# Optimization experiments

Measured on AMD Instinct MI355X. Metric: run time of the kernel, lower is better.

The kernel has to match this reference:

```python
import jax, jax.numpy as jnp
import numpy as np
from jax import lax

SHARED = 512
THRESH = 1.0   # LifNeuron threshold from source
DECAY = 0.9    # assumed LIF membrane decay (LifNeuron source not provided)


def spike(u):
    return (u >= 0.0).astype(u.dtype)


def lif(x):
    # Leaky integrate-and-fire over the time axis. x: (B, T, D) -> spikes (B, T, D)
    def step(mem, xt):
        mem = DECAY * mem + xt
        s = spike(mem - THRESH)
        return mem - s * THRESH, s
    x_t = jnp.swapaxes(x, 0, 1)  # (T, B, D)
    _, spikes = lax.scan(step, jnp.zeros((x.shape[0], x.shape[2]), x.dtype), x_t)
    return jnp.swapaxes(spikes, 0, 1)


def setup_inputs() -> dict:
    key = jax.random.key(0)
    ks = jax.random.split(key, 10)
    B, T, S = 2, 32, 64
    Dv, Da = 768, 512
    TENSOR_DIM = (SHARED + 1) ** 2  # 263169

    def lin_w(k, fan_in, fan_out):
        # torch.nn.Linear default init scale ~ 1/sqrt(fan_in)
        return (jax.random.normal(k, (fan_out, fan_in), jnp.float32)
                * np.float32(1.0 / np.sqrt(fan_in)))

    return {
        "vision": jax.random.uniform(ks[0], (B, T, S, Dv), jnp.float32),
        "audio": jax.random.uniform(ks[1], (B, T, S, Da), jnp.float32),
        "vw1": lin_w(ks[2], Dv, SHARED), "vb1": jnp.zeros((SHARED,), jnp.float32),
        "vw2": lin_w(ks[3], SHARED, SHARED), "vb2": jnp.zeros((SHARED,), jnp.float32),
        "aw1": lin_w(ks[4], Da, SHARED), "ab1": jnp.zeros((SHARED,), jnp.float32),
        "aw2": lin_w(ks[5], SHARED, SHARED), "ab2": jnp.zeros((SHARED,), jnp.float32),
        "fw1": lin_w(ks[6], TENSOR_DIM, 2 * SHARED), "fb1": jnp.zeros((2 * SHARED,), jnp.float32),
        "fw2": lin_w(ks[7], 2 * SHARED, SHARED), "fb2": jnp.zeros((SHARED,), jnp.float32),
    }


def reference(vision, audio, vw1, vb1, vw2, vb2, aw1, ab1, aw2, ab2,
              fw1, fb1, fw2, fb2):
    def unimodal(x, w1, b1, w2, b2):
        p = x.mean(axis=2)  # (B, T, D_mod) - pool over spike/token axis
        h = jax.nn.relu(jnp.einsum('btd,hd->bth', p, w1) + b1)
        h = jnp.einsum('bth,oh->bto', h, w2) + b2  # (B, T, SHARED)
        ones = jnp.ones(h.shape[:-1] + (1,), h.dtype)
        return jnp.concatenate([h, ones], axis=-1)  # (B, T, SHARED+1)

    a = unimodal(vision, vw1, vb1, vw2, vb2)
    b = unimodal(audio, aw1, ab1, aw2, ab2)
    B, T, _ = a.shape
    # outer-product tensor fusion: (B, T, (SHARED+1)^2)
    tp = jnp.einsum('btd,bte->btde', a, b).reshape(B, T, -1)
    h = jax.nn.relu(jnp.einsum('btk,ok->bto', tp, fw1) + fb1)
    fused = jnp.einsum('bto,fo->btf', h, fw2) + fb2  # (B, T, SHARED)
    return lif(fused)
```

## Files before the change

### kernel.cpp

```cpp
#include <hip/hip_runtime.h>

#define AB 513
#define TD 263169
#define TILE 16416

typedef float f4 __attribute__((ext_vector_type(4)));
typedef float f32x4 __attribute__((ext_vector_type(4)));
typedef short bf16x8 __attribute__((ext_vector_type(8)));
typedef int i32x4 __attribute__((ext_vector_type(4)));
#define GAS __attribute__((address_space(1)))
#define LAS __attribute__((address_space(3)))

__global__ __launch_bounds__(256) void pool_kernel(
    const float* __restrict__ vx, const float* __restrict__ ax,
    float* __restrict__ pvT, float* __restrict__ paT)
{
    const int isA = (blockIdx.x >= 64);
    const int bt = blockIdx.x & 63;
    const float* x = isA ? ax : vx;
    float* pT = isA ? paT : pvT;
    const int D = isA ? 512 : 768;
    const int nd4 = D >> 2;
    const int tid = threadIdx.x;
    if (tid < nd4) {
        f4 s0 = {0.f, 0.f, 0.f, 0.f}, s1 = s0, s2 = s0, s3 = s0;
        const float* xp = x + (size_t)bt * 64 * D + tid * 4;
        #pragma unroll 4
        for (int ss = 0; ss < 64; ss += 4) {
            s0 += *(const f4*)(xp + (size_t)ss * D);
            s1 += *(const f4*)(xp + (size_t)(ss + 1) * D);
            s2 += *(const f4*)(xp + (size_t)(ss + 2) * D);
            s3 += *(const f4*)(xp + (size_t)(ss + 3) * D);
        }
        const f4 s = ((s0 + s1) + (s2 + s3)) * 0.015625f;
        #pragma unroll
        for (int q = 0; q < 4; ++q) pT[(tid * 4 + q) * 64 + bt] = s[q];
    }
}

__global__ __launch_bounds__(512) void mlp1_kernel(
    const float* __restrict__ pvT, const float* __restrict__ paT,
    const float* __restrict__ vw1, const float* __restrict__ vb1,
    const float* __restrict__ aw1, const float* __restrict__ ab1,
    float* __restrict__ h1vT, float* __restrict__ h1aT)
{
    const int isA = (blockIdx.x >= 64);
    const int D = isA ? 512 : 768;
    const float* pT = isA ? paT : pvT;
    const float* w1 = isA ? aw1 : vw1;
    const float* b1 = isA ? ab1 : vb1;
    float* h1T = isA ? h1aT : h1vT;
    const int tid = threadIdx.x, lane = tid & 63, w = tid >> 6;
    const int h = (blockIdx.x & 63) * 8 + w;
    const float* wr = w1 + (size_t)h * D;

    float a0 = 0.f, a1 = 0.f, a2 = 0.f, a3 = 0.f;
    for (int d = 0; d < D; d += 16) {
        const f4 w0 = *(const f4*)(wr + d);
        const f4 w1v = *(const f4*)(wr + d + 4);
        const f4 w2v = *(const f4*)(wr + d + 8);
        const f4 w3v = *(const f4*)(wr + d + 12);
        #pragma unroll
        for (int q = 0; q < 4; ++q) {
            a0 = fmaf(w0[q],  pT[(d + q) * 64 + lane], a0);
            a1 = fmaf(w1v[q], pT[(d + 4 + q) * 64 + lane], a1);
            a2 = fmaf(w2v[q], pT[(d + 8 + q) * 64 + lane], a2);
            a3 = fmaf(w3v[q], pT[(d + 12 + q) * 64 + lane], a3);
        }
    }
    h1T[h * 64 + lane] = fmaxf((a0 + a1) + (a2 + a3) + b1[h], 0.f);
}

__global__ __launch_bounds__(512) void mlp2_kernel(
    const float* __restrict__ h1vT, const float* __restrict__ h1aT,
    const float* __restrict__ vw2, const float* __restrict__ vb2,
    const float* __restrict__ aw2, const float* __restrict__ ab2,
    float* __restrict__ aTout, float* __restrict__ bTout)
{
    const int isA = (blockIdx.x >= 64);
    const float* hT = isA ? h1aT : h1vT;
    const float* w2 = isA ? aw2 : vw2;
    const float* b2 = isA ? ab2 : vb2;
    float* outT = isA ? bTout : aTout;
    const int tid = threadIdx.x, lane = tid & 63, w = tid >> 6;
    const int h = (blockIdx.x & 63) * 8 + w;
    const float* wr = w2 + (size_t)h * 512;

    float a0 = 0.f, a1 = 0.f, a2 = 0.f, a3 = 0.f;
    for (int d = 0; d < 512; d += 16) {
        const f4 w0 = *(const f4*)(wr + d);
        const f4 w1v = *(const f4*)(wr + d + 4);
        const f4 w2v = *(const f4*)(wr + d + 8);
        const f4 w3v = *(const f4*)(wr + d + 12);
        #pragma unroll
        for (int q = 0; q < 4; ++q) {
            a0 = fmaf(w0[q],  hT[(d + q) * 64 + lane], a0);
            a1 = fmaf(w1v[q], hT[(d + 4 + q) * 64 + lane], a1);
            a2 = fmaf(w2v[q], hT[(d + 8 + q) * 64 + lane], a2);
            a3 = fmaf(w3v[q], hT[(d + 12 + q) * 64 + lane], a3);
        }
    }
    outT[h * 64 + lane] = (a0 + a1) + (a2 + a3) + b2[h];
    if ((blockIdx.x & 63) == 0 && tid < 64) outT[512 * 64 + tid] = 1.0f;
}

__global__ __launch_bounds__(256) void aprep_kernel(
    const float* __restrict__ aT,
    short* __restrict__ aF1, short* __restrict__ aF2, short* __restrict__ aF3)
{
    const int t = blockIdx.x * 256 + threadIdx.x;
    const int l = t & 63, mt = (t >> 6) & 3, kt = t >> 8;
    const int m = mt * 16 + (l & 15);
    const int kbase = kt * 32 + ((l >> 4) << 3);
    const int obase = ((kt * 4 + mt) * 64 + l) * 8;
    #pragma unroll
    for (int i = 0; i < 8; ++i) {
        const float v = aT[(size_t)(kbase + i) * 64 + m];
        const unsigned u = __float_as_uint(v);
        const float r1 = v - __uint_as_float(u & 0xFFFF0000u);
        const unsigned u1 = __float_as_uint(r1);
        const float r2 = r1 - __uint_as_float(u1 & 0xFFFF0000u);
        const unsigned u2 = __float_as_uint(r2);
        aF1[obase + i] = (short)(u >> 16);
        aF2[obase + i] = (short)(u1 >> 16);
        aF3[obase + i] = (short)(u2 >> 16);
    }
}

__global__ __launch_bounds__(512, 1) void bilinear_kernel(
    const float* __restrict__ fw1,
    const float* __restrict__ fb1,
    const float* __restrict__ aT,
    const float* __restrict__ bT,
    const short* __restrict__ aF1, const short* __restrict__ aF2,
    const short* __restrict__ aF3,
    float* __restrict__ hbufT)
{
    __shared__ float lds[33344];
    float* const buf0 = lds;
    float* const buf1 = lds + 16448;
    float* const ldsdump = lds + 32896;

    const int tid = threadIdx.x;
    const int l = tid & 63, w = tid >> 6;
    const int o = blockIdx.x;
    const float* __restrict__ W = fw1 + (size_t)o * TD;
    const int we0 = w * 64;
    const int lq = l >> 4, ln = l & 15;

    #define STAGE(bufb_, c_)                                                   \
        do {                                                                   \
            const float* csrc_ = W + (size_t)(c_) * TILE;                      \
            _Pragma("unroll")                                                  \
            for (int is_ = 0; is_ < 8; ++is_) {                                \
                __builtin_amdgcn_global_load_lds(                              \
                    (const GAS unsigned*)(const void*)(csrc_ + w * 2048 + is_ * 256 + l * 4), \
                    (LAS unsigned*)(void*)((bufb_) + w * 2048 + is_ * 256), 16, 0, 0); \
            }                                                                  \
            {       \
                const float* rs_ = csrc_ + 16384 + (l & 31);                   \
                float* rd_ = (w == 0) ? ((bufb_) + 16384) : (ldsdump + (w - 1) * 64); \
                __builtin_amdgcn_global_load_lds(                              \
                    (const GAS unsigned*)(const void*)rs_,                     \
                    (LAS unsigned*)(void*)rd_, 4, 0, 0);                       \
            }                                                                  \
        } while (0)

    #define LOADA(A1r, A2r, A3r, kt_)                                          \
        do {                                                                   \
            _Pragma("unroll")                                                  \
            for (int mt_ = 0; mt_ < 4; ++mt_) {                                \
                const int fb_ = (((kt_) * 4 + mt_) * 64 + l) * 8;              \
                A1r[mt_] = *(const bf16x8*)(aF1 + fb_);                        \
                A2r[mt_] = *(const bf16x8*)(aF2 + fb_);                        \
                A3r[mt_] = *(const bf16x8*)(aF3 + fb_);                        \
            }                                                                  \
        } while (0)

    #define COMPUTE(wb_, A1r, A2r, A3r)                                        \
        do {                                                                   \
            _Pragma("unroll")                                                  \
            for (int nt = 0; nt < 4; ++nt) {                                   \
                unsigned u0[8], u1[8], u2[8];                                  \
                _Pragma("unroll")                                              \
                for (int i = 0; i < 8; ++i) {                                  \
                    const float v = (wb_)[(lq * 8 + i) * 513 + we0 + nt * 16 + ln]; \
                    u0[i] = __float_as_uint(v);                                \
                    const float r1 = v - __uint_as_float(u0[i] & 0xFFFF0000u); \
                    u1[i] = __float_as_uint(r1);                               \
                    const float r2 = r1 - __uint_as_float(u1[i] & 0xFFFF0000u);\
                    u2[i] = __float_as_uint(r2);                               \
                }                                                              \
                i32x4 p1, p2, p3;                                              \
                _Pragma("unroll")                                              \
                for (int j = 0; j < 4; ++j) {                                  \
                    p1[j] = (int)((u0[2 * j + 1] & 0xFFFF0000u) | (u0[2 * j] >> 16)); \
                    p2[j] = (int)((u1[2 * j + 1] & 0xFFFF0000u) | (u1[2 * j] >> 16)); \
                    p3[j] = (int)((u2[2 * j + 1] & 0xFFFF0000u) | (u2[2 * j] >> 16)); \
                }                                                              \
                const bf16x8 B1 = __builtin_bit_cast(bf16x8, p1);              \
                const bf16x8 B2 = __builtin_bit_cast(bf16x8, p2);              \
                const bf16x8 B3 = __builtin_bit_cast(bf16x8, p3);              \
                _Pragma("unroll")                                              \
                for (int mt = 0; mt < 4; ++mt) {                               \
                    acc[mt][nt] = __builtin_amdgcn_mfma_f32_16x16x32_bf16(A1r[mt], B1, acc[mt][nt], 0, 0, 0); \
                    acc[mt][nt] = __builtin_amdgcn_mfma_f32_16x16x32_bf16(A1r[mt], B2, acc[mt][nt], 0, 0, 0); \
                    acc[mt][nt] = __builtin_amdgcn_mfma_f32_16x16x32_bf16(A2r[mt], B1, acc[mt][nt], 0, 0, 0); \
                    acc[mt][nt] = __builtin_amdgcn_mfma_f32_16x16x32_bf16(A2r[mt], B2, acc[mt][nt], 0, 0, 0); \
                    acc[mt][nt] = __builtin_amdgcn_mfma_f32_16x16x32_bf16(A1r[mt], B3, acc[mt][nt], 0, 0, 0); \
                    acc[mt][nt] = __builtin_amdgcn_mfma_f32_16x16x32_bf16(A3r[mt], B1, acc[mt][nt], 0, 0, 0); \
                }                                                              \
            }                                                                  \
        } while (0)

    f32x4 acc[4][4];
    #pragma unroll
    for (int mt = 0; mt < 4; ++mt)
        #pragma unroll
        for (int nt = 0; nt < 4; ++nt)
            acc[mt][nt] = (f32x4){0.f, 0.f, 0.f, 0.f};

    bf16x8 Aa1[4], Aa2[4], Aa3[4], Ab1[4], Ab2[4], Ab3[4];

    STAGE(buf0, 0);
    LOADA(Aa1, Aa2, Aa3, 0);
    STAGE(buf1, 1);

    #pragma unroll 1
    for (int it = 0; it < 7; ++it) {
        asm volatile("s_waitcnt vmcnt(9)" ::: "memory");
        __builtin_amdgcn_s_barrier();
        LOADA(Ab1, Ab2, Ab3, 2 * it + 1);
        COMPUTE(buf0, Aa1, Aa2, Aa3);
        __builtin_amdgcn_s_barrier();
        STAGE(buf0, 2 * it + 2);

        asm volatile("s_waitcnt vmcnt(9)" ::: "memory");
        __builtin_amdgcn_s_barrier();
        LOADA(Aa1, Aa2, Aa3, 2 * it + 2);
        COMPUTE(buf1, Ab1, Ab2, Ab3);
        __builtin_amdgcn_s_barrier();
        STAGE(buf1, 2 * it + 3);
    }
    asm volatile("s_waitcnt vmcnt(9)" ::: "memory");
    __builtin_amdgcn_s_barrier();
    LOADA(Ab1, Ab2, Ab3, 15);
    COMPUTE(buf0, Aa1, Aa2, Aa3);
    __builtin_amdgcn_s_barrier();
    asm volatile("s_waitcnt vmcnt(0)" ::: "memory");
    __builtin_amdgcn_s_barrier();
    COMPUTE(buf1, Ab1, Ab2, Ab3);

    float ysum[4][4];
    #pragma unroll
    for (int mt = 0; mt < 4; ++mt)
        #pragma unroll
        for (int r = 0; r < 4; ++r) ysum[mt][r] = 0.f;
    #pragma unroll
    for (int mt = 0; mt < 4; ++mt) {
        const int bt0 = mt * 16 + lq * 4;
        #pragma unroll
        for (int nt = 0; nt < 4; ++nt) {
            const int e = we0 + nt * 16 + ln;
            const f4 bv = *(const f4*)(bT + (size_t)e * 64 + bt0);
            #pragma unroll
            for (int r = 0; r < 4; ++r)
                ysum[mt][r] = fmaf(acc[mt][nt][r], bv[r], ysum[mt][r]);
        }
    }
    #pragma unroll
    for (int mt = 0; mt < 4; ++mt)
        #pragma unroll
        for (int r = 0; r < 4; ++r) {
            float v = ysum[mt][r];
            v += __shfl_xor(v, 1, 64);
            v += __shfl_xor(v, 2, 64);
            v += __shfl_xor(v, 4, 64);
            v += __shfl_xor(v, 8, 64);
            ysum[mt][r] = v;
        }
    __syncthreads();
    if (ln == 0) {
        #pragma unroll
        for (int mt = 0; mt < 4; ++mt)
            #pragma unroll
            for (int r = 0; r < 4; ++r)
                buf0[w * 64 + mt * 16 + lq * 4 + r] = ysum[mt][r];
    }

    {
        float s0 = 0.f, s1 = 0.f, s2 = 0.f, s3 = 0.f;
        #pragma unroll 4
        for (int k = 0; k < 64; k += 4) {
            s0 = fmaf(aT[(size_t)(we0 + k) * 64 + l], W[(size_t)(we0 + k) * AB + 512], s0);
            s1 = fmaf(aT[(size_t)(we0 + k + 1) * 64 + l], W[(size_t)(we0 + k + 1) * AB + 512], s1);
            s2 = fmaf(aT[(size_t)(we0 + k + 2) * 64 + l], W[(size_t)(we0 + k + 2) * AB + 512], s2);
            s3 = fmaf(aT[(size_t)(we0 + k + 3) * 64 + l], W[(size_t)(we0 + k + 3) * AB + 512], s3);
        }
        #pragma unroll 4
        for (int k = 0; k < 64; k += 4) {
            s0 = fmaf(W[(size_t)512 * AB + we0 + k], bT[(size_t)(we0 + k) * 64 + l], s0);
            s1 = fmaf(W[(size_t)512 * AB + we0 + k + 1], bT[(size_t)(we0 + k + 1) * 64 + l], s1);
            s2 = fmaf(W[(size_t)512 * AB + we0 + k + 2], bT[(size_t)(we0 + k + 2) * 64 + l], s2);
            s3 = fmaf(W[(size_t)512 * AB + we0 + k + 3], bT[(size_t)(we0 + k + 3) * 64 + l], s3);
        }
        buf0[512 + w * 64 + l] = (s0 + s1) + (s2 + s3);
    }

    __syncthreads();

    if (w == 0) {
        float t2 = 0.f;
        #pragma unroll
        for (int k = 0; k < 8; ++k)
            t2 += buf0[k * 64 + l] + buf0[512 + k * 64 + l];
        t2 += W[(size_t)512 * AB + 512] + fb1[o];
        hbufT[(size_t)o * 64 + l] = fmaxf(t2, 0.f);
    }
    #undef STAGE
    #undef LOADA
    #undef COMPUTE
}

__global__ __launch_bounds__(512) void fuse2_kernel(
    const float* __restrict__ hbufT,
    const float* __restrict__ fw2,
    const float* __restrict__ fb2,
    float* __restrict__ fused)
{
    const int tid = threadIdx.x, lane = tid & 63, w = tid >> 6;
    #pragma unroll
    for (int k = 0; k < 2; ++k) {
        const int f = blockIdx.x * 16 + w * 2 + k;
        const float* wr = fw2 + (size_t)f * 1024;
        float a0 = 0.f, a1 = 0.f, a2 = 0.f, a3 = 0.f;
        for (int o = 0; o < 1024; o += 16) {
            const f4 w0 = *(const f4*)(wr + o);
            const f4 w1v = *(const f4*)(wr + o + 4);
            const f4 w2v = *(const f4*)(wr + o + 8);
            const f4 w3v = *(const f4*)(wr + o + 12);
            #pragma unroll
            for (int q = 0; q < 4; ++q) {
                a0 = fmaf(w0[q],  hbufT[(o + q) * 64 + lane], a0);
                a1 = fmaf(w1v[q], hbufT[(o + 4 + q) * 64 + lane], a1);
                a2 = fmaf(w2v[q], hbufT[(o + 8 + q) * 64 + lane], a2);
                a3 = fmaf(w3v[q], hbufT[(o + 12 + q) * 64 + lane], a3);
            }
        }
        fused[lane * 512 + f] = (a0 + a1) + (a2 + a3) + fb2[f];
    }
}

__global__ __launch_bounds__(256) void lif_kernel(
    const float* __restrict__ fused,
    float* __restrict__ out)
{
    const int idx = blockIdx.x * 256 + threadIdx.x;
    if (idx >= 1024) return;
    const int b = idx >> 9, dd = idx & 511;
    float mem = 0.f;
    for (int t = 0; t < 32; ++t) {
        const size_t off = ((size_t)(b * 32 + t) * 512) + dd;
        mem = 0.9f * mem + fused[off];
        const float s = (mem >= 1.0f) ? 1.0f : 0.0f;
        out[off] = s;
        mem -= s;
    }
}

extern "C" void kernel_launch(void* const* d_in, const int* in_sizes, int n_in,
                              void* d_out, int out_size, void* d_ws, size_t ws_size,
                              hipStream_t stream) {
    const float* vision = (const float*)d_in[0];
    const float* audio  = (const float*)d_in[1];
    const float* vw1 = (const float*)d_in[2];
    const float* vb1 = (const float*)d_in[3];
    const float* vw2 = (const float*)d_in[4];
    const float* vb2 = (const float*)d_in[5];
    const float* aw1 = (const float*)d_in[6];
    const float* ab1 = (const float*)d_in[7];
    const float* aw2 = (const float*)d_in[8];
    const float* ab2 = (const float*)d_in[9];
    const float* fw1 = (const float*)d_in[10];
    const float* fb1 = (const float*)d_in[11];
    const float* fw2 = (const float*)d_in[12];
    const float* fb2 = (const float*)d_in[13];
    float* out = (float*)d_out;

    float* ws    = (float*)d_ws;
    float* pvT   = ws;
    float* paT   = pvT + 768 * 64;
    float* h1vT  = paT + 512 * 64;
    float* h1aT  = h1vT + 512 * 64;
    float* aT    = h1aT + 512 * 64;
    float* bT    = aT + AB * 64;
    float* hbufT = bT + AB * 64;
    float* fused = hbufT + 1024 * 64;
    short* aF1   = (short*)(fused + 64 * 512);
    short* aF2   = aF1 + 32768;
    short* aF3   = aF2 + 32768;

    pool_kernel<<<128, 256, 0, stream>>>(vision, audio, pvT, paT);
    mlp1_kernel<<<128, 512, 0, stream>>>(pvT, paT, vw1, vb1, aw1, ab1, h1vT, h1aT);
    mlp2_kernel<<<128, 512, 0, stream>>>(h1vT, h1aT, vw2, vb2, aw2, ab2, aT, bT);
    aprep_kernel<<<16, 256, 0, stream>>>(aT, aF1, aF2, aF3);
    bilinear_kernel<<<1024, 512, 0, stream>>>(fw1, fb1, aT, bT, aF1, aF2, aF3, hbufT);
    fuse2_kernel<<<32, 512, 0, stream>>>(hbufT, fw2, fb2, fused);
    lif_kernel<<<4, 256, 0, stream>>>(fused, out);
}
```

Measured before the change: 423.2 us.

## Pipeline bilinear kernel with triple-buffered LDS ring for weights and A fragments

```diff
diff --git a/kernel.cpp b/kernel.cpp
--- a/kernel.cpp
+++ b/kernel.cpp
@@ -2,7 +2,6 @@
 
 #define AB 513
 #define TD 263169
-#define TILE 16416
 
 typedef float f4 __attribute__((ext_vector_type(4)));
 typedef float f32x4 __attribute__((ext_vector_type(4)));
@@ -15,27 +14,21 @@
     const float* __restrict__ vx, const float* __restrict__ ax,
     float* __restrict__ pvT, float* __restrict__ paT)
 {
-    const int isA = (blockIdx.x >= 64);
-    const int bt = blockIdx.x & 63;
-    const float* x = isA ? ax : vx;
-    float* pT = isA ? paT : pvT;
-    const int D = isA ? 512 : 768;
-    const int nd4 = D >> 2;
-    const int tid = threadIdx.x;
-    if (tid < nd4) {
-        f4 s0 = {0.f, 0.f, 0.f, 0.f}, s1 = s0, s2 = s0, s3 = s0;
-        const float* xp = x + (size_t)bt * 64 * D + tid * 4;
-        #pragma unroll 4
-        for (int ss = 0; ss < 64; ss += 4) {
-            s0 += *(const f4*)(xp + (size_t)ss * D);
-            s1 += *(const f4*)(xp + (size_t)(ss + 1) * D);
-            s2 += *(const f4*)(xp + (size_t)(ss + 2) * D);
-            s3 += *(const f4*)(xp + (size_t)(ss + 3) * D);
-        }
-        const f4 s = ((s0 + s1) + (s2 + s3)) * 0.015625f;
-        #pragma unroll
-        for (int q = 0; q < 4; ++q) pT[(tid * 4 + q) * 64 + bt] = s[q];
-    }
+    int b = blockIdx.x;
+    const float* x; float* pT; int D, bt, dc;
+    if (b < 192) { x = vx; pT = pvT; D = 768; bt = b / 3; dc = b % 3; }
+    else { b -= 192; x = ax; pT = paT; D = 512; bt = b >> 1; dc = b & 1; }
+    const int d = dc * 256 + threadIdx.x;
+    const float* xp = x + (size_t)bt * 64 * D + d;
+    float s0 = 0.f, s1 = 0.f, s2 = 0.f, s3 = 0.f;
+    #pragma unroll 4
+    for (int ss = 0; ss < 64; ss += 4) {
+        s0 += xp[(size_t)ss * D];
+        s1 += xp[(size_t)(ss + 1) * D];
+        s2 += xp[(size_t)(ss + 2) * D];
+        s3 += xp[(size_t)(ss + 3) * D];
+    }
+    pT[d * 64 + bt] = ((s0 + s1) + (s2 + s3)) * 0.015625f;
 }
 
 __global__ __launch_bounds__(512) void mlp1_kernel(
@@ -106,13 +99,13 @@
 
 __global__ __launch_bounds__(256) void aprep_kernel(
     const float* __restrict__ aT,
-    short* __restrict__ aF1, short* __restrict__ aF2, short* __restrict__ aF3)
+    short* __restrict__ aFc)
 {
     const int t = blockIdx.x * 256 + threadIdx.x;
     const int l = t & 63, mt = (t >> 6) & 3, kt = t >> 8;
     const int m = mt * 16 + (l & 15);
     const int kbase = kt * 32 + ((l >> 4) << 3);
-    const int obase = ((kt * 4 + mt) * 64 + l) * 8;
+    const int cb = kt * 12 + mt * 3;
     #pragma unroll
     for (int i = 0; i < 8; ++i) {
         const float v = aT[(size_t)(kbase + i) * 64 + m];
@@ -121,9 +114,9 @@
         const unsigned u1 = __float_as_uint(r1);
         const float r2 = r1 - __uint_as_float(u1 & 0xFFFF0000u);
         const unsigned u2 = __float_as_uint(r2);
-        aF1[obase + i] = (short)(u >> 16);
-        aF2[obase + i] = (short)(u1 >> 16);
-        aF3[obase + i] = (short)(u2 >> 16);
+        aFc[((size_t)(cb + 0) * 64 + l) * 8 + i] = (short)(u >> 16);
+        aFc[((size_t)(cb + 1) * 64 + l) * 8 + i] = (short)(u1 >> 16);
+        aFc[((size_t)(cb + 2) * 64 + l) * 8 + i] = (short)(u2 >> 16);
     }
 }
 
@@ -132,59 +125,74 @@
     const float* __restrict__ fb1,
     const float* __restrict__ aT,
     const float* __restrict__ bT,
-    const short* __restrict__ aF1, const short* __restrict__ aF2,
-    const short* __restrict__ aF3,
+    const short* __restrict__ aFc,
     float* __restrict__ hbufT)
 {
-    __shared__ float lds[33344];
-    float* const buf0 = lds;
-    float* const buf1 = lds + 16448;
-    float* const ldsdump = lds + 32896;
+    __shared__ float wring[3][8192];
+    __shared__ short aring[3][6144];
+    __shared__ float adump[256];
 
     const int tid = threadIdx.x;
     const int l = tid & 63, w = tid >> 6;
     const int o = blockIdx.x;
     const float* __restrict__ W = fw1 + (size_t)o * TD;
-    const int we0 = w * 64;
     const int lq = l >> 4, ln = l & 15;
 
-    #define STAGE(bufb_, c_)                                                   \
+    #define STAGE_W(e_)                                                        \
         do {                                                                   \
-            const float* csrc_ = W + (size_t)(c_) * TILE;                      \
+            const int ee_ = (e_), kt_ = ee_ >> 1, eh_ = ee_ & 1, en_ = ee_ % 3;\
             _Pragma("unroll")                                                  \
-            for (int is_ = 0; is_ < 8; ++is_) {                                \
+            for (int rr_ = 0; rr_ < 4; ++rr_) {                                \
+                const int r_ = w * 4 + rr_;                                    \
                 __builtin_amdgcn_global_load_lds(                              \
-                    (const GAS unsigned*)(const void*)(csrc_ + w * 2048 + is_ * 256 + l * 4), \
-                    (LAS unsigned*)(void*)((bufb_) + w * 2048 + is_ * 256), 16, 0, 0); \
-            }                                                                  \
-            {       \
-                const float* rs_ = csrc_ + 16384 + (l & 31);                   \
-                float* rd_ = (w == 0) ? ((bufb_) + 16384) : (ldsdump + (w - 1) * 64); \
-                __builtin_amdgcn_global_load_lds(                              \
-                    (const GAS unsigned*)(const void*)rs_,                     \
-                    (LAS unsigned*)(void*)rd_, 4, 0, 0);                       \
+                    (const GAS unsigned*)(const void*)(W + (size_t)(kt_ * 32 + r_) * AB + 256 * eh_ + l * 4), \
+                    (LAS unsigned*)(void*)(&wring[en_][r_ * 256]), 16, 0, 0);  \
             }                                                                  \
         } while (0)
 
-    #define LOADA(A1r, A2r, A3r, kt_)                                          \
+    #define STAGE_A(kt_)                                                       \
         do {                                                                   \
+            const int kk_ = (kt_), en_ = kk_ % 3;                              \
+            const int c0_ = (w < 4) ? (2 * w) : (4 + w);                       \
+            const short* s0_ = aFc + ((size_t)kk_ * 12 + c0_) * 512;           \
+            __builtin_amdgcn_global_load_lds(                                  \
+                (const GAS unsigned*)(const void*)(s0_ + l * 8),               \
+                (LAS unsigned*)(void*)(&aring[en_][c0_ * 512]), 16, 0, 0);     \
+            if (w < 4) {                                                       \
+                const int c1_ = 2 * w + 1;                                     \
+                const short* s1_ = aFc + ((size_t)kk_ * 12 + c1_) * 512;       \
+                __builtin_amdgcn_global_load_lds(                              \
+                    (const GAS unsigned*)(const void*)(s1_ + l * 8),           \
+                    (LAS unsigned*)(void*)(&aring[en_][c1_ * 512]), 16, 0, 0); \
+            } else {                                                           \
+                const short* s1_ = aFc + (size_t)kk_ * 12 * 512;               \
+                __builtin_amdgcn_global_load_lds(                              \
+                    (const GAS unsigned*)(const void*)(s1_ + l * 2),           \
+                    (LAS unsigned*)(void*)(adump), 4, 0, 0);                   \
+            }                                                                  \
+        } while (0)
+
+    #define LOADA_LDS(kt_)                                                     \
+        do {                                                                   \
+            const int en_ = (kt_) % 3;                                         \
             _Pragma("unroll")                                                  \
             for (int mt_ = 0; mt_ < 4; ++mt_) {                                \
-                const int fb_ = (((kt_) * 4 + mt_) * 64 + l) * 8;              \
-                A1r[mt_] = *(const bf16x8*)(aF1 + fb_);                        \
-                A2r[mt_] = *(const bf16x8*)(aF2 + fb_);                        \
-                A3r[mt_] = *(const bf16x8*)(aF3 + fb_);                        \
+                A1[mt_] = *(const bf16x8*)&aring[en_][(mt_ * 3 + 0) * 512 + l * 8]; \
+                A2[mt_] = *(const bf16x8*)&aring[en_][(mt_ * 3 + 1) * 512 + l * 8]; \
+                A3[mt_] = *(const bf16x8*)&aring[en_][(mt_ * 3 + 2) * 512 + l * 8]; \
             }                                                                  \
         } while (0)
 
-    #define COMPUTE(wb_, A1r, A2r, A3r)                                        \
+    #define COMPUTE(e_, EHC)                                                   \
         do {                                                                   \
+            const float* __restrict__ wb_ = &wring[(e_) % 3][0];               \
             _Pragma("unroll")                                                  \
-            for (int nt = 0; nt < 4; ++nt) {                                   \
+            for (int ntl = 0; ntl < 2; ++ntl) {                                \
+                const int col_ = 32 * w + 16 * ntl + ln;                       \
                 unsigned u0[8], u1[8], u2[8];                                  \
                 _Pragma("unroll")                                              \
                 for (int i = 0; i < 8; ++i) {                                  \
-                    const float v = (wb_)[(lq * 8 + i) * 513 + we0 + nt * 16 + ln]; \
+                    const float v = wb_[(lq * 8 + i) * 256 + col_];            \
                     u0[i] = __float_as_uint(v);                                \
                     const float r1 = v - __uint_as_float(u0[i] & 0xFFFF0000u); \
                     u1[i] = __float_as_uint(r1);                               \
@@ -203,12 +211,12 @@
                 const bf16x8 B3 = __builtin_bit_cast(bf16x8, p3);              \
                 _Pragma("unroll")                                              \
                 for (int mt = 0; mt < 4; ++mt) {                               \
-                    acc[mt][nt] = __builtin_amdgcn_mfma_f32_16x16x32_bf16(A1r[mt], B1, acc[mt][nt], 0, 0, 0); \
-                    acc[mt][nt] = __builtin_amdgcn_mfma_f32_16x16x32_bf16(A1r[mt], B2, acc[mt][nt], 0, 0, 0); \
-                    acc[mt][nt] = __builtin_amdgcn_mfma_f32_16x16x32_bf16(A2r[mt], B1, acc[mt][nt], 0, 0, 0); \
-                    acc[mt][nt] = __builtin_amdgcn_mfma_f32_16x16x32_bf16(A2r[mt], B2, acc[mt][nt], 0, 0, 0); \
-                    acc[mt][nt] = __builtin_amdgcn_mfma_f32_16x16x32_bf16(A1r[mt], B3, acc[mt][nt], 0, 0, 0); \
-                    acc[mt][nt] = __builtin_amdgcn_mfma_f32_16x16x32_bf16(A3r[mt], B1, acc[mt][nt], 0, 0, 0); \
+                    acc[mt][(EHC) * 2 + ntl] = __builtin_amdgcn_mfma_f32_16x16x32_bf16(A1[mt], B1, acc[mt][(EHC) * 2 + ntl], 0, 0, 0); \
+                    acc[mt][(EHC) * 2 + ntl] = __builtin_amdgcn_mfma_f32_16x16x32_bf16(A1[mt], B2, acc[mt][(EHC) * 2 + ntl], 0, 0, 0); \
+                    acc[mt][(EHC) * 2 + ntl] = __builtin_amdgcn_mfma_f32_16x16x32_bf16(A2[mt], B1, acc[mt][(EHC) * 2 + ntl], 0, 0, 0); \
+                    acc[mt][(EHC) * 2 + ntl] = __builtin_amdgcn_mfma_f32_16x16x32_bf16(A2[mt], B2, acc[mt][(EHC) * 2 + ntl], 0, 0, 0); \
+                    acc[mt][(EHC) * 2 + ntl] = __builtin_amdgcn_mfma_f32_16x16x32_bf16(A1[mt], B3, acc[mt][(EHC) * 2 + ntl], 0, 0, 0); \
+                    acc[mt][(EHC) * 2 + ntl] = __builtin_amdgcn_mfma_f32_16x16x32_bf16(A3[mt], B1, acc[mt][(EHC) * 2 + ntl], 0, 0, 0); \
                 }                                                              \
             }                                                                  \
         } while (0)
@@ -219,37 +227,31 @@
         #pragma unroll
         for (int nt = 0; nt < 4; ++nt)
             acc[mt][nt] = (f32x4){0.f, 0.f, 0.f, 0.f};
-
-    bf16x8 Aa1[4], Aa2[4], Aa3[4], Ab1[4], Ab2[4], Ab3[4];
-
-    STAGE(buf0, 0);
-    LOADA(Aa1, Aa2, Aa3, 0);
-    STAGE(buf1, 1);
+    bf16x8 A1[4], A2[4], A3[4];
+
+    STAGE_W(0);
+    STAGE_A(0);
+    STAGE_W(1);
+    STAGE_A(1);
 
     #pragma unroll 1
-    for (int it = 0; it < 7; ++it) {
-        asm volatile("s_waitcnt vmcnt(9)" ::: "memory");
+    for (int kt = 0; kt < 16; ++kt) {
+        const int e0 = 2 * kt;
+        asm volatile("s_waitcnt vmcnt(6)" ::: "memory");
         __builtin_amdgcn_s_barrier();
-        LOADA(Ab1, Ab2, Ab3, 2 * it + 1);
-        COMPUTE(buf0, Aa1, Aa2, Aa3);
+        LOADA_LDS(kt);
+        COMPUTE(e0, 0);
         __builtin_amdgcn_s_barrier();
-        STAGE(buf0, 2 * it + 2);
-
-        asm volatile("s_waitcnt vmcnt(9)" ::: "memory");
+        STAGE_W(e0 + 2 <= 31 ? e0 + 2 : 31);
+        STAGE_A(kt + 2 <= 15 ? kt + 2 : 15);
+        asm volatile("s_waitcnt vmcnt(6)" ::: "memory");
         __builtin_amdgcn_s_barrier();
-        LOADA(Aa1, Aa2, Aa3, 2 * it + 2);
-        COMPUTE(buf1, Ab1, Ab2, Ab3);
+        COMPUTE(e0 + 1, 1);
         __builtin_amdgcn_s_barrier();
-        STAGE(buf1, 2 * it + 3);
-    }
-    asm volatile("s_waitcnt vmcnt(9)" ::: "memory");
-    __builtin_amdgcn_s_barrier();
-    LOADA(Ab1, Ab2, Ab3, 15);
-    COMPUTE(buf0, Aa1, Aa2, Aa3);
-    __builtin_amdgcn_s_barrier();
+        STAGE_W(e0 + 3 <= 31 ? e0 + 3 : 31);
+    }
     asm volatile("s_waitcnt vmcnt(0)" ::: "memory");
     __builtin_amdgcn_s_barrier();
-    COMPUTE(buf1, Ab1, Ab2, Ab3);
 
     float ysum[4][4];
     #pragma unroll
@@ -260,12 +262,12 @@
     for (int mt = 0; mt < 4; ++mt) {
         const int bt0 = mt * 16 + lq * 4;
         #pragma unroll
-        for (int nt = 0; nt < 4; ++nt) {
-            const int e = we0 + nt * 16 + ln;
+        for (int ntg = 0; ntg < 4; ++ntg) {
+            const int e = 256 * (ntg >> 1) + 32 * w + 16 * (ntg & 1) + ln;
             const f4 bv = *(const f4*)(bT + (size_t)e * 64 + bt0);
             #pragma unroll
             for (int r = 0; r < 4; ++r)
-                ysum[mt][r] = fmaf(acc[mt][nt][r], bv[r], ysum[mt][r]);
+                ysum[mt][r] = fmaf(acc[mt][ntg][r], bv[r], ysum[mt][r]);
         }
     }
     #pragma unroll
@@ -279,16 +281,16 @@
             v += __shfl_xor(v, 8, 64);
             ysum[mt][r] = v;
         }
-    __syncthreads();
     if (ln == 0) {
         #pragma unroll
         for (int mt = 0; mt < 4; ++mt)
             #pragma unroll
             for (int r = 0; r < 4; ++r)
-                buf0[w * 64 + mt * 16 + lq * 4 + r] = ysum[mt][r];
+                wring[0][w * 64 + mt * 16 + lq * 4 + r] = ysum[mt][r];
     }
 
     {
+        const int we0 = w * 64;
         float s0 = 0.f, s1 = 0.f, s2 = 0.f, s3 = 0.f;
         #pragma unroll 4
         for (int k = 0; k < 64; k += 4) {
@@ -304,7 +306,7 @@
             s2 = fmaf(W[(size_t)512 * AB + we0 + k + 2], bT[(size_t)(we0 + k + 2) * 64 + l], s2);
             s3 = fmaf(W[(size_t)512 * AB + we0 + k + 3], bT[(size_t)(we0 + k + 3) * 64 + l], s3);
         }
-        buf0[512 + w * 64 + l] = (s0 + s1) + (s2 + s3);
+        wring[0][512 + w * 64 + l] = (s0 + s1) + (s2 + s3);
     }
 
     __syncthreads();
@@ -313,12 +315,13 @@
         float t2 = 0.f;
         #pragma unroll
         for (int k = 0; k < 8; ++k)
-            t2 += buf0[k * 64 + l] + buf0[512 + k * 64 + l];
+            t2 += wring[0][k * 64 + l] + wring[0][512 + k * 64 + l];
         t2 += W[(size_t)512 * AB + 512] + fb1[o];
         hbufT[(size_t)o * 64 + l] = fmaxf(t2, 0.f);
     }
-    #undef STAGE
-    #undef LOADA
+    #undef STAGE_W
+    #undef STAGE_A
+    #undef LOADA_LDS
     #undef COMPUTE
 }
 
@@ -396,15 +399,13 @@
     float* bT    = aT + AB * 64;
     float* hbufT = bT + AB * 64;
     float* fused = hbufT + 1024 * 64;
-    short* aF1   = (short*)(fused + 64 * 512);
-    short* aF2   = aF1 + 32768;
-    short* aF3   = aF2 + 32768;
-
-    pool_kernel<<<128, 256, 0, stream>>>(vision, audio, pvT, paT);
+    short* aFc   = (short*)(fused + 64 * 512);
+
+    pool_kernel<<<320, 256, 0, stream>>>(vision, audio, pvT, paT);
     mlp1_kernel<<<128, 512, 0, stream>>>(pvT, paT, vw1, vb1, aw1, ab1, h1vT, h1aT);
     mlp2_kernel<<<128, 512, 0, stream>>>(h1vT, h1aT, vw2, vb2, aw2, ab2, aT, bT);
-    aprep_kernel<<<16, 256, 0, stream>>>(aT, aF1, aF2, aF3);
-    bilinear_kernel<<<1024, 512, 0, stream>>>(fw1, fb1, aT, bT, aF1, aF2, aF3, hbufT);
+    aprep_kernel<<<16, 256, 0, stream>>>(aT, aFc);
+    bilinear_kernel<<<1024, 512, 0, stream>>>(fw1, fb1, aT, bT, aFc, hbufT);
     fuse2_kernel<<<32, 512, 0, stream>>>(hbufT, fw2, fb2, fused);
     lif_kernel<<<4, 256, 0, stream>>>(fused, out);
 }
```

Result: slower. 440.8 us (+4.2%).
